# Kernel tuning notes

Hardware: AMD Instinct MI355X
Metric: run time of the kernel (lower is better)

Reference implementation:

```python
import jax, jax.numpy as jnp
import numpy as np

DX = 1.0  # voxel_spacing

def _grad(t, axis):
    """Central difference along `axis` with replicate (Neumann) boundaries.
    Matches F.pad(mode='replicate') + conv3d with a +/-0.5 stencil."""
    pad = [(0, 0)] * t.ndim
    pad[axis] = (1, 1)
    p = jnp.pad(t, pad, mode='edge')
    n = p.shape[axis]
    fwd = jax.lax.slice_in_dim(p, 2, n, axis=axis)
    bwd = jax.lax.slice_in_dim(p, 0, n - 2, axis=axis)
    return (fwd - bwd) * (0.5 / DX)

# axis mapping for [B, C, D, H, W]: grad_x -> W (4), grad_y -> H (3), grad_z -> D (2)
_AXES = (4, 3, 2)

def setup_inputs() -> dict:
    key = jax.random.key(0)
    k1, k2, k3 = jax.random.split(key, 3)
    shape = (4, 1, 192, 192, 192)
    u = jax.random.uniform(k1, shape, dtype=jnp.float32)
    D = jax.random.uniform(k2, shape, dtype=jnp.float32)
    rho = jax.random.uniform(k3, shape, dtype=jnp.float32)
    return {"u": u, "D": D, "rho": rho}

def reference(u, D, rho):
    # div(D * grad(u))
    div = jnp.zeros_like(u)
    for ax in _AXES:
        flux = D * _grad(u, ax)
        div = div + _grad(flux, ax)
    # du/dt = div(D grad u) + rho * u * (1 - u)
    return div + rho * u * (1.0 - u)
```

## Files before the change

kernel.cpp:

```cpp
#include <hip/hip_runtime.h>


#define NX 192

__global__ __launch_bounds__(192)
void fk_kernel(const float* __restrict__ u,
               const float* __restrict__ Dd,
               const float* __restrict__ rho,
               float* __restrict__ out)
{
    const int x = threadIdx.x;
    int row = blockIdx.x;
    const int y = row % NX;
    row /= NX;
    const int z = row % NX;
    const int b = row / NX;

    const int base = ((b * NX + z) * NX + y) * NX + x;

    const float uc = u[base];

    auto divterm = [&](int c, int stride) -> float {
        const int n = NX;
        const int jp  = (c + 1 < n) ? (c + 1) : (n - 1);
        const int jm  = (c - 1 > 0) ? (c - 1) : 0;
        const int jpp = (jp + 1 < n) ? (jp + 1) : (n - 1);
        const int jpm = jp - 1;
        const int jmp = jm + 1;
        const int jmm = (jm - 1 > 0) ? (jm - 1) : 0;

        const float fp = Dd[base + (jp - c) * stride] *
                         (u[base + (jpp - c) * stride] - u[base + (jpm - c) * stride]);
        const float fm = Dd[base + (jm - c) * stride] *
                         (u[base + (jmp - c) * stride] - u[base + (jmm - c) * stride]);
        return (fp - fm) * 0.25f;
    };

    const float dx = divterm(x, 1);
    const float dy = divterm(y, NX);
    const float dz = divterm(z, NX * NX);

    const float reaction = rho[base] * uc * (1.0f - uc);

    out[base] = dx + dy + dz + reaction;
}

extern "C" void kernel_launch(void* const* d_in, const int* in_sizes, int n_in,
                              void* d_out, int out_size, void* d_ws, size_t ws_size,
                              hipStream_t stream) {
    const float* u   = (const float*)d_in[0];
    const float* Dd  = (const float*)d_in[1];
    const float* rho = (const float*)d_in[2];
    float* out = (float*)d_out;

    const int B = 4;
    const int rows = B * NX * NX;

    fk_kernel<<<rows, NX, 0, stream>>>(u, Dd, rho, out);
}
```

Before: 125.8 us.

## Tile stencil into shared-memory slabs with z-marching and register prefetch

Replaces the one-thread-per-voxel kernel, which issued many redundant global loads per point, with 64x16 xy tiles that march through 24-deep z chunks. Haloed u and D planes go into rotating shared-memory slabs, and the next plane is prefetched into registers while the current one is computed. Each thread produces four x-adjacent outputs using float4 accesses, with z-neighbors carried in registers. This cuts repeated global and cache traffic, at the cost of more complex boundary handling, a per-plane barrier, and a small grid of 1152 blocks.

```diff
diff --git a/kernel.cpp b/kernel.cpp
--- a/kernel.cpp
+++ b/kernel.cpp
@@ -1,48 +1,235 @@
 #include <hip/hip_runtime.h>
 
 
-#define NX 192
-
-__global__ __launch_bounds__(192)
+#define NX    192
+#define SP    (NX * NX)
+#define ZC    24
+#define LROW  72
+#define UROWS 20
+#define DROWS 18
+#define USLAB (UROWS * LROW)
+#define DSLAB (DROWS * LROW)
+#define NTHR  256
+#define UPAIRS (USLAB / 2)
+#define DPAIRS (DSLAB / 2)
+
+#define LD4(p, o) (*(const float4*)((p) + (o)))
+
+__global__ __launch_bounds__(NTHR, 4)
 void fk_kernel(const float* __restrict__ u,
                const float* __restrict__ Dd,
                const float* __restrict__ rho,
                float* __restrict__ out)
 {
-    const int x = threadIdx.x;
-    int row = blockIdx.x;
-    const int y = row % NX;
-    row /= NX;
-    const int z = row % NX;
-    const int b = row / NX;
-
-    const int base = ((b * NX + z) * NX + y) * NX + x;
-
-    const float uc = u[base];
-
-    auto divterm = [&](int c, int stride) -> float {
-        const int n = NX;
-        const int jp  = (c + 1 < n) ? (c + 1) : (n - 1);
-        const int jm  = (c - 1 > 0) ? (c - 1) : 0;
-        const int jpp = (jp + 1 < n) ? (jp + 1) : (n - 1);
-        const int jpm = jp - 1;
-        const int jmp = jm + 1;
-        const int jmm = (jm - 1 > 0) ? (jm - 1) : 0;
-
-        const float fp = Dd[base + (jp - c) * stride] *
-                         (u[base + (jpp - c) * stride] - u[base + (jpm - c) * stride]);
-        const float fm = Dd[base + (jm - c) * stride] *
-                         (u[base + (jmp - c) * stride] - u[base + (jmm - c) * stride]);
-        return (fp - fm) * 0.25f;
-    };
-
-    const float dx = divterm(x, 1);
-    const float dy = divterm(y, NX);
-    const float dz = divterm(z, NX * NX);
-
-    const float reaction = rho[base] * uc * (1.0f - uc);
-
-    out[base] = dx + dy + dz + reaction;
+    __shared__ float Ush[4 * USLAB];
+    __shared__ float Dsh[3 * DSLAB];
+
+    const int tx  = threadIdx.x;
+    const int ty  = threadIdx.y;
+    const int tid = ty * 16 + tx;
+
+    int bid = blockIdx.x;
+    const int xt = bid % 3;  bid /= 3;
+    const int yt = bid % 12; bid /= 12;
+    const int zc = bid % 8;  bid /= 8;
+    const int b  = bid;
+
+    const int x0 = xt * 64, y0 = yt * 16, z0 = zc * ZC;
+
+    const size_t vol = (size_t)b * NX * SP;
+    const float* ub = u   + vol;
+    const float* db = Dd  + vol;
+    const float* rb = rho + vol;
+    float*       ob = out + vol;
+
+    int  uoff[3], doff[3];
+    bool uedge[3], dedge[3];
+    bool uact[3], dact[3];
+    #pragma unroll
+    for (int k = 0; k < 3; ++k) {
+        {
+            const int p = tid + NTHR * k;
+            uact[k] = (p < UPAIRS);
+            const int pp = uact[k] ? p : 0;
+            const int r = pp / (LROW / 2), pc = pp % (LROW / 2);
+            int gy = y0 + r - 2; gy = gy < 0 ? 0 : (gy > NX - 1 ? NX - 1 : gy);
+            const int gx0 = x0 + 2 * pc - 4;
+            const bool e = (gx0 < 0) || (gx0 > NX - 2);
+            const int gxc = (gx0 < 0) ? 0 : NX - 1;
+            uoff[k]  = gy * NX + (e ? gxc : gx0);
+            uedge[k] = e;
+        }
+        {
+            const int p = tid + NTHR * k;
+            dact[k] = (p < DPAIRS);
+            const int pp = dact[k] ? p : 0;
+            const int r = pp / (LROW / 2), pc = pp % (LROW / 2);
+            int gy = y0 + r - 1; gy = gy < 0 ? 0 : (gy > NX - 1 ? NX - 1 : gy);
+            const int gx0 = x0 + 2 * pc - 4;
+            const bool e = (gx0 < 0) || (gx0 > NX - 2);
+            const int gxc = (gx0 < 0) ? 0 : NX - 1;
+            doff[k]  = gy * NX + (e ? gxc : gx0);
+            dedge[k] = e;
+        }
+    }
+
+    auto stageU = [&](const float* pl, float2* s) {
+        #pragma unroll
+        for (int k = 0; k < 3; ++k) if (uact[k]) {
+            if (!uedge[k]) s[k] = *(const float2*)(pl + uoff[k]);
+            else { const float f = pl[uoff[k]]; s[k] = make_float2(f, f); }
+        }
+    };
+    auto stageD = [&](const float* pl, float2* s) {
+        #pragma unroll
+        for (int k = 0; k < 3; ++k) if (dact[k]) {
+            if (!dedge[k]) s[k] = *(const float2*)(pl + doff[k]);
+            else { const float f = pl[doff[k]]; s[k] = make_float2(f, f); }
+        }
+    };
+    auto writeU = [&](float* slab, const float2* s) {
+        #pragma unroll
+        for (int k = 0; k < 3; ++k) if (uact[k])
+            *(float2*)(slab + 2 * (tid + NTHR * k)) = s[k];
+    };
+    auto writeD = [&](float* slab, const float2* s) {
+        #pragma unroll
+        for (int k = 0; k < 3; ++k) if (dact[k])
+            *(float2*)(slab + 2 * (tid + NTHR * k)) = s[k];
+    };
+
+    {
+        float2 s[3];
+        #pragma unroll
+        for (int sI = 0; sI < 3; ++sI) {
+            stageU(ub + (size_t)(z0 + sI) * SP, s);
+            writeU(Ush + sI * USLAB, s);
+        }
+        #pragma unroll
+        for (int sI = 0; sI < 2; ++sI) {
+            stageD(db + (size_t)(z0 + sI) * SP, s);
+            writeD(Dsh + sI * DSLAB, s);
+        }
+    }
+
+    const int x = x0 + 4 * tx, y = y0 + ty;
+    const size_t gcen = (size_t)y * NX + x;
+
+    const int zm1 = (z0 - 1 > 0) ? z0 - 1 : 0;
+    const int zm2 = (z0 - 2 > 0) ? z0 - 2 : 0;
+    float4 um1  = LD4(ub, (size_t)zm1 * SP + gcen);
+    float4 um2  = LD4(ub, (size_t)zm2 * SP + gcen);
+    float4 dm1  = LD4(db, (size_t)zm1 * SP + gcen);
+    float4 rcur = LD4(rb, (size_t)z0 * SP + gcen);
+
+    const int ubl = (ty + 2) * LROW + (4 * tx + 4);
+    const int dbl = (ty + 1) * LROW + (4 * tx + 4);
+
+    const bool fx0 = (x == 0);
+    const bool fx3 = (x + 3 == NX - 1);
+    const bool fy0 = (y == 0);
+    const bool fy1 = (y == NX - 1);
+
+    __syncthreads();
+
+    int su0 = 0, su1 = 1, su2 = 2, su3 = 3;
+    int sd0 = 0, sd1 = 1, sd2 = 2;
+
+    for (int iz = 0; iz < ZC; ++iz) {
+        const int z  = z0 + iz;
+        const bool pf = (iz + 1 < ZC);
+
+        float2 uS[3], dS[3];
+        float4 rnx;
+        if (pf) {
+            const int zu = (z + 3 > NX - 1) ? NX - 1 : z + 3;
+            const int zd = (z + 2 > NX - 1) ? NX - 1 : z + 2;
+            stageU(ub + (size_t)zu * SP, uS);
+            stageD(db + (size_t)zd * SP, dS);
+            rnx = LD4(rb, (size_t)(z + 1) * SP + gcen);
+        }
+
+        const float* Uc = Ush + su0 * USLAB;
+        const float* Dc = Dsh + sd0 * DSLAB;
+        const float4 uxm4 = LD4(Uc, ubl - 4);
+        const float4 ucc  = LD4(Uc, ubl);
+        const float4 uxp4 = LD4(Uc, ubl + 4);
+        const float4 dxm4 = LD4(Dc, dbl - 4);
+        const float4 dcc  = LD4(Dc, dbl);
+        const float4 dxp4 = LD4(Dc, dbl + 4);
+        const float4 uym2 = LD4(Uc, ubl - 2 * LROW);
+        const float4 uyp2 = LD4(Uc, ubl + 2 * LROW);
+        const float4 dym  = LD4(Dc, dbl - LROW);
+        const float4 dyp  = LD4(Dc, dbl + LROW);
+        const float4 uzp2 = LD4(Ush + su2 * USLAB, ubl);
+        const float4 dzp  = LD4(Dsh + sd1 * DSLAB, dbl);
+
+        const float w8[8] = {uxm4.z, uxm4.w, ucc.x, ucc.y, ucc.z, ucc.w, uxp4.x, uxp4.y};
+        const float d6[6] = {dxm4.w, dcc.x, dcc.y, dcc.z, dcc.w, dxp4.x};
+        float divx[4];
+        #pragma unroll
+        for (int i = 0; i < 4; ++i)
+            divx[i] = d6[i + 2] * (w8[i + 4] - w8[i + 2]) - d6[i] * (w8[i + 2] - w8[i]);
+        if (fx0) divx[0] = d6[2] * (w8[4] - w8[2]) - d6[1] * (w8[3] - w8[2]);
+        if (fx3) divx[3] = d6[4] * (w8[5] - w8[4]) - d6[3] * (w8[5] - w8[3]);
+
+        float4 divy;
+        if (fy0) {
+            const float4 uyp1 = LD4(Uc, ubl + LROW);
+            divy.x = dyp.x * (uyp2.x - ucc.x) - dym.x * (uyp1.x - ucc.x);
+            divy.y = dyp.y * (uyp2.y - ucc.y) - dym.y * (uyp1.y - ucc.y);
+            divy.z = dyp.z * (uyp2.z - ucc.z) - dym.z * (uyp1.z - ucc.z);
+            divy.w = dyp.w * (uyp2.w - ucc.w) - dym.w * (uyp1.w - ucc.w);
+        } else if (fy1) {
+            const float4 uym1 = LD4(Uc, ubl - LROW);
+            divy.x = dyp.x * (ucc.x - uym1.x) - dym.x * (ucc.x - uym2.x);
+            divy.y = dyp.y * (ucc.y - uym1.y) - dym.y * (ucc.y - uym2.y);
+            divy.z = dyp.z * (ucc.z - uym1.z) - dym.z * (ucc.z - uym2.z);
+            divy.w = dyp.w * (ucc.w - uym1.w) - dym.w * (ucc.w - uym2.w);
+        } else {
+            divy.x = dyp.x * (uyp2.x - ucc.x) - dym.x * (ucc.x - uym2.x);
+            divy.y = dyp.y * (uyp2.y - ucc.y) - dym.y * (ucc.y - uym2.y);
+            divy.z = dyp.z * (uyp2.z - ucc.z) - dym.z * (ucc.z - uym2.z);
+            divy.w = dyp.w * (uyp2.w - ucc.w) - dym.w * (ucc.w - uym2.w);
+        }
+
+        float4 divz;
+        if (z == 0) {
+            const float4 uzp1 = LD4(Ush + su1 * USLAB, ubl);
+            divz.x = dzp.x * (uzp2.x - ucc.x) - dm1.x * (uzp1.x - ucc.x);
+            divz.y = dzp.y * (uzp2.y - ucc.y) - dm1.y * (uzp1.y - ucc.y);
+            divz.z = dzp.z * (uzp2.z - ucc.z) - dm1.z * (uzp1.z - ucc.z);
+            divz.w = dzp.w * (uzp2.w - ucc.w) - dm1.w * (uzp1.w - ucc.w);
+        } else if (z == NX - 1) {
+            divz.x = dzp.x * (ucc.x - um1.x) - dm1.x * (ucc.x - um2.x);
+            divz.y = dzp.y * (ucc.y - um1.y) - dm1.y * (ucc.y - um2.y);
+            divz.z = dzp.z * (ucc.z - um1.z) - dm1.z * (ucc.z - um2.z);
+            divz.w = dzp.w * (ucc.w - um1.w) - dm1.w * (ucc.w - um2.w);
+        } else {
+            divz.x = dzp.x * (uzp2.x - ucc.x) - dm1.x * (ucc.x - um2.x);
+            divz.y = dzp.y * (uzp2.y - ucc.y) - dm1.y * (ucc.y - um2.y);
+            divz.z = dzp.z * (uzp2.z - ucc.z) - dm1.z * (ucc.z - um2.z);
+            divz.w = dzp.w * (uzp2.w - ucc.w) - dm1.w * (ucc.w - um2.w);
+        }
+
+        float4 o;
+        o.x = 0.25f * (divx[0] + divy.x + divz.x) + rcur.x * ucc.x * (1.0f - ucc.x);
+        o.y = 0.25f * (divx[1] + divy.y + divz.y) + rcur.y * ucc.y * (1.0f - ucc.y);
+        o.z = 0.25f * (divx[2] + divy.z + divz.z) + rcur.z * ucc.z * (1.0f - ucc.z);
+        o.w = 0.25f * (divx[3] + divy.w + divz.w) + rcur.w * ucc.w * (1.0f - ucc.w);
+        *(float4*)(ob + (size_t)z * SP + gcen) = o;
+
+        um2 = um1; um1 = ucc; dm1 = dcc;
+
+        if (pf) {
+            writeU(Ush + su3 * USLAB, uS);
+            writeD(Dsh + sd2 * DSLAB, dS);
+            __syncthreads();
+            int t = su0; su0 = su1; su1 = su2; su2 = su3; su3 = t;
+            t = sd0; sd0 = sd1; sd1 = sd2; sd2 = t;
+            rcur = rnx;
+        }
+    }
 }
 
 extern "C" void kernel_launch(void* const* d_in, const int* in_sizes, int n_in,
@@ -53,8 +240,7 @@
     const float* rho = (const float*)d_in[2];
     float* out = (float*)d_out;
 
-    const int B = 4;
-    const int rows = B * NX * NX;
-
-    fk_kernel<<<rows, NX, 0, stream>>>(u, Dd, rho, out);
+    dim3 block(16, 16, 1);
+    const int grid = 3 * 12 * 8 * 4;
+    fk_kernel<<<grid, block, 0, stream>>>(u, Dd, rho, out);
 }
```

Measured after the change: 156.9 us. +24.7%, slower.
